# Kernel optimization log

Hardware: AMD Instinct MI355X
Metric: run time of the kernel (lower is better)

## Reference

```python
import jax, jax.numpy as jnp
import numpy as np

N = 50000
H = 300


def l2_normalize(x, eps=1e-12):
    n = jnp.sqrt(jnp.sum(x * x, axis=1, keepdims=True))
    return x / jnp.maximum(n, eps)


def gat_layer(x, ei_j, ei_i, a_i, a_j, n_nodes):
    # per-node scalar scores, gathered per edge
    s_i = x @ a_i  # [N]
    s_j = x @ a_j  # [N]
    e = jax.nn.leaky_relu(s_i[ei_i] + s_j[ei_j], 0.01)  # [E]
    # scatter softmax over incoming edges of node i
    m = jax.ops.segment_max(e, ei_i, num_segments=n_nodes)
    ex = jnp.exp(e - m[ei_i])
    denom = jax.ops.segment_sum(ex, ei_i, num_segments=n_nodes)
    alpha = ex / (denom[ei_i] + 1e-16)
    out = jax.ops.segment_sum(alpha[:, None] * x[ei_j], ei_i, num_segments=n_nodes)
    return jax.nn.relu(out)


def gcn_layer(x, ei_j, ei_i, W, n_nodes):
    deg = jax.ops.segment_sum(jnp.ones_like(ei_i, dtype=x.dtype), ei_i, num_segments=n_nodes)
    dinv = jnp.where(deg > 0, deg ** -0.5, 0.0)
    norm = dinv[ei_j] * dinv[ei_i]  # [E]
    h = x @ W.T
    out = jax.ops.segment_sum(norm[:, None] * h[ei_j], ei_i, num_segments=n_nodes)
    return jax.nn.relu(out)


def highway(x1, x2, W, b):
    gate = jax.nn.sigmoid(x1 @ W.T + b)
    return gate * x2 + (1.0 - gate) * x1


def setup_inputs() -> dict:
    key = jax.random.key(0)
    ks = jax.random.split(key, 16)
    s = 1.0 / np.sqrt(H)
    inp = {
        "x_e": jax.random.normal(ks[0], (N, H), dtype=jnp.float32),
        "edge_index": jax.random.randint(ks[1], (2, 400000), 0, N, dtype=jnp.int32),
        "rel": jax.random.randint(ks[2], (400000,), 0, 1000, dtype=jnp.int32),
        "edge_index_all": jax.random.randint(ks[3], (2, 800000), 0, N, dtype=jnp.int32),
        "rel_all": jax.random.randint(ks[4], (800000,), 0, 1000, dtype=jnp.int32),
        "gcn1_W": jax.random.uniform(ks[5], (H, H), jnp.float32, -s, s),
        "hw1_W": jax.random.uniform(ks[6], (H, H), jnp.float32, -s, s),
        "hw1_b": jax.random.uniform(ks[7], (H,), jnp.float32, -s, s),
        "gat1_ai": jax.random.uniform(ks[8], (H,), jnp.float32, -s, s),
        "gat1_aj": jax.random.uniform(ks[9], (H,), jnp.float32, -s, s),
        "ghw1_W": jax.random.uniform(ks[10], (H, H), jnp.float32, -s, s),
        "ghw1_b": jax.random.uniform(ks[11], (H,), jnp.float32, -s, s),
        "gat2_ai": jax.random.uniform(ks[12], (H,), jnp.float32, -s, s),
        "gat2_aj": jax.random.uniform(ks[13], (H,), jnp.float32, -s, s),
        "ghw2_W": jax.random.uniform(ks[14], (H, H), jnp.float32, -s, s),
        "ghw2_b": jax.random.uniform(ks[15], (H,), jnp.float32, -s, s),
    }
    k2 = jax.random.split(jax.random.key(1), 2)
    inp["gat_ai"] = jax.random.uniform(k2[0], (H,), jnp.float32, -s, s)
    inp["gat_aj"] = jax.random.uniform(k2[1], (H,), jnp.float32, -s, s)
    return inp


def reference(x_e, edge_index, rel, edge_index_all, rel_all,
              gcn1_W, hw1_W, hw1_b, gat1_ai, gat1_aj, ghw1_W, ghw1_b,
              gat2_ai, gat2_aj, ghw2_W, ghw2_b, gat_ai, gat_aj):
    # dropout(p=0.05) treated as identity (eval mode)
    ei_j, ei_i = edge_index_all[0], edge_index_all[1]
    n = x_e.shape[0]

    x0 = l2_normalize(x_e)
    x2 = highway(x0, gcn_layer(x0, ei_j, ei_i, gcn1_W, n), hw1_W, hw1_b)
    x3 = highway(x2, gat_layer(x2, ei_j, ei_i, gat1_ai, gat1_aj, n), ghw1_W, ghw1_b)
    xe = highway(x2, gat_layer(x3, ei_j, ei_i, gat2_ai, gat2_aj, n), ghw2_W, ghw2_b)
    ye = gat_layer(xe, ei_j, ei_i, gat_ai, gat_aj, n)
    return jnp.concatenate([xe, ye], axis=1)
```

## Files before the change

kernel.cpp:

```cpp
#include <hip/hip_runtime.h>
#include <hip/hip_bf16.h>
#include <math.h>

#define H 300
#define WAVE 64
#define STRB 320
#define NCP 20
#define NSS 12
#define ACT 240
#define SCB 1024

typedef short bf16x8 __attribute__((ext_vector_type(8)));
typedef unsigned short u16;
typedef u16 u16x8 __attribute__((ext_vector_type(8)));
typedef u16 u16x4 __attribute__((ext_vector_type(4)));
typedef float f32x4 __attribute__((ext_vector_type(4)));

__device__ inline unsigned short f2b(float f) {
    union { float f; unsigned int u; } x; x.f = f;
    unsigned int r = x.u + 0x7FFF + ((x.u >> 16) & 1);
    return (unsigned short)(r >> 16);
}
__device__ inline float b2f(u16 h) {
    union { float f; unsigned int u; } x; x.u = ((unsigned int)h) << 16;
    return x.f;
}

__global__ void k_l2norm(const float* __restrict__ x, u16* __restrict__ outb, int n) {
    int wave = blockIdx.x * (blockDim.x / WAVE) + (threadIdx.x >> 6);
    int lane = threadIdx.x & 63;
    if (wave >= n) return;
    const float* row = x + (long)wave * H;
    float s = 0.f;
    for (int j = lane; j < H; j += WAVE) { float v = row[j]; s += v * v; }
    for (int o = 32; o > 0; o >>= 1) s += __shfl_xor(s, o);
    float sc = 1.0f / fmaxf(sqrtf(s), 1e-12f);
    u16* brow = outb + (long)wave * STRB;
    for (int j = lane; j < H; j += WAVE) brow[j] = f2b(row[j] * sc);
    for (int j = H + lane; j < STRB; j += WAVE) brow[j] = 0;
}

__global__ void k_zero_int(int* p, int n) {
    int i = blockIdx.x * blockDim.x + threadIdx.x;
    int stride = gridDim.x * blockDim.x;
    for (; i < n; i += stride) p[i] = 0;
}

__global__ void k_count_deg(const int* __restrict__ ei_i, int* __restrict__ deg, int E) {
    int i = blockIdx.x * blockDim.x + threadIdx.x;
    int stride = gridDim.x * blockDim.x;
    for (; i < E; i += stride) atomicAdd(&deg[ei_i[i]], 1);
}

__global__ void k_dinv(const int* __restrict__ deg, float* __restrict__ dinv, int n) {
    int i = blockIdx.x * blockDim.x + threadIdx.x;
    int stride = gridDim.x * blockDim.x;
    for (; i < n; i += stride) {
        int d = deg[i];
        dinv[i] = (d > 0) ? 1.0f / sqrtf((float)d) : 0.0f;
    }
}

__global__ void k_scan_local(const int* __restrict__ deg, int* __restrict__ offs,
                             int* __restrict__ btot, int n) {
    __shared__ int sh[SCB];
    int base = blockIdx.x * SCB;
    int tid = threadIdx.x;
    int v = (base + tid < n) ? deg[base + tid] : 0;
    sh[tid] = v;
    __syncthreads();
    for (int off = 1; off < SCB; off <<= 1) {
        int add = (tid >= off) ? sh[tid - off] : 0;
        __syncthreads();
        sh[tid] += add;
        __syncthreads();
    }
    if (base + tid < n) offs[base + tid] = sh[tid] - v;
    if (tid == SCB - 1) btot[blockIdx.x] = sh[tid];
}

__global__ void k_scan_tots(const int* __restrict__ btot, int* __restrict__ bpre,
                            int nb, int* __restrict__ total_out) {
    int l = threadIdx.x;
    int v = (l < nb) ? btot[l] : 0;
    int own = v;
    for (int o = 1; o < 64; o <<= 1) {
        int u = __shfl_up(v, o);
        if (l >= o) v += u;
    }
    if (l < nb) bpre[l] = v - own;
    if (l == 63) total_out[0] = v;
}

__global__ void k_scan_apply(int* __restrict__ offs, const int* __restrict__ bpre,
                             int* __restrict__ cursor, int n) {
    int i = blockIdx.x * blockDim.x + threadIdx.x;
    int stride = gridDim.x * blockDim.x;
    for (; i < n; i += stride) {
        int o = offs[i] + bpre[i / SCB];
        offs[i] = o;
        cursor[i] = o;
    }
}

__global__ void k_fill_csr(const int* __restrict__ ei_j, const int* __restrict__ ei_i,
                           int* __restrict__ cursor, int* __restrict__ csr_src, int E) {
    int i = blockIdx.x * blockDim.x + threadIdx.x;
    int stride = gridDim.x * blockDim.x;
    for (; i < E; i += stride) {
        int dst = ei_i[i];
        int pos = atomicAdd(&cursor[dst], 1);
        csr_src[pos] = ei_j[i];
    }
}

__global__ void k_conv_w(const float* __restrict__ W, u16* __restrict__ Wb) {
    int idx = blockIdx.x * blockDim.x + threadIdx.x;
    int stride = gridDim.x * blockDim.x;
    for (; idx < STRB * STRB; idx += stride) {
        int r = idx / STRB, c = idx - r * STRB;
        Wb[idx] = (r < H && c < H) ? f2b(W[r * H + c]) : 0;
    }
}

#define BM 128
#define BN 64
#define BK 32
#define LDP 40
#define NXCD 8

__global__ __launch_bounds__(256) void k_gemm_fused(
        const u16* __restrict__ Xb,
        const u16* __restrict__ Wb,
        u16* __restrict__ outb,
        const float* __restrict__ hwbias,
        const u16* __restrict__ xnewb, const float* __restrict__ xnewf,
        const u16* __restrict__ xold,
        float* __restrict__ outf, long ostride,
        u16* __restrict__ mirror,
        int n_rows) {
    __shared__ __align__(16) short As[BM * LDP];
    __shared__ __align__(16) short Bs[BN * LDP];
    const int tid = threadIdx.x;

    const int nwg = gridDim.x;
    const int q = nwg / NXCD, r = nwg % NXCD;
    const int xcd = blockIdx.x % NXCD, idx = blockIdx.x / NXCD;
    const int wgid = (xcd < r ? xcd * (q + 1) : r * (q + 1) + (xcd - r) * q) + idx;
    const int bm = (wgid / 5) * BM;
    const int bn = (wgid % 5) * BN;

    const int lane = tid & 63;
    const int wid = tid >> 6;
    const int wr = wid >> 1;
    const int wc = wid & 1;
    const int lrow = lane & 15;
    const int kgrp = lane >> 4;

    f32x4 acc[4][2];
    #pragma unroll
    for (int m = 0; m < 4; m++)
        #pragma unroll
        for (int n = 0; n < 2; n++) acc[m][n] = (f32x4){0.f, 0.f, 0.f, 0.f};

    for (int k0 = 0; k0 < STRB; k0 += BK) {
        #pragma unroll
        for (int i = 0; i < 2; ++i) {
            int qq = tid + i * 256;
            int rr = qq >> 2, c = (qq & 3) << 3;
            int gr = bm + rr;
            u16x8 v = {0, 0, 0, 0, 0, 0, 0, 0};
            if (gr < n_rows) v = *(const u16x8*)&Xb[(long)gr * STRB + k0 + c];
            *(u16x8*)&As[rr * LDP + c] = v;
        }
        {
            int rr = tid >> 2, c = (tid & 3) << 3;
            u16x8 v = *(const u16x8*)&Wb[(long)(bn + rr) * STRB + k0 + c];
            *(u16x8*)&Bs[rr * LDP + c] = v;
        }
        __syncthreads();

        bf16x8 af[4], bfr[2];
        #pragma unroll
        for (int m = 0; m < 4; m++) {
            int row = wr * 64 + m * 16 + lrow;
            af[m] = *(const bf16x8*)&As[row * LDP + kgrp * 8];
        }
        #pragma unroll
        for (int n = 0; n < 2; n++) {
            int col = wc * 32 + n * 16 + lrow;
            bfr[n] = *(const bf16x8*)&Bs[col * LDP + kgrp * 8];
        }
        #pragma unroll
        for (int m = 0; m < 4; m++)
            #pragma unroll
            for (int n = 0; n < 2; n++)
                acc[m][n] = __builtin_amdgcn_mfma_f32_16x16x32_bf16(af[m], bfr[n], acc[m][n], 0, 0, 0);
        __syncthreads();
    }

    if (outb) {
        #pragma unroll
        for (int m = 0; m < 4; m++)
            #pragma unroll
            for (int n = 0; n < 2; n++) {
                int gc = bn + wc * 32 + n * 16 + lrow;
                if (gc >= STRB) continue;
                #pragma unroll
                for (int rr = 0; rr < 4; rr++) {
                    int gr = bm + wr * 64 + m * 16 + kgrp * 4 + rr;
                    if (gr < n_rows) outb[(long)gr * STRB + gc] = (gc < H) ? f2b(acc[m][n][rr]) : 0;
                }
            }
    } else {
        #pragma unroll
        for (int m = 0; m < 4; m++)
            #pragma unroll
            for (int n = 0; n < 2; n++) {
                int gc = bn + wc * 32 + n * 16 + lrow;
                if (gc >= STRB) continue;
                bool colv = (gc < H);
                float bb = colv ? hwbias[gc] : 0.f;
                #pragma unroll
                for (int rr = 0; rr < 4; rr++) {
                    int gr = bm + wr * 64 + m * 16 + kgrp * 4 + rr;
                    if (gr >= n_rows) continue;
                    if (colv) {
                        float pre = acc[m][n][rr] + bb;
                        float g = 1.0f / (1.0f + __expf(-pre));
                        float xn = xnewb ? b2f(xnewb[(long)gr * STRB + gc])
                                         : xnewf[(long)gr * H + gc];
                        float xo = b2f(xold[(long)gr * STRB + gc]);
                        float val = g * xn + (1.0f - g) * xo;
                        if (outf) outf[(long)gr * ostride + gc] = val;
                        if (mirror) mirror[(long)gr * STRB + gc] = f2b(val);
                    } else if (mirror) {
                        mirror[(long)gr * STRB + gc] = 0;
                    }
                }
            }
    }
}

__global__ __launch_bounds__(256) void k_gcn_gather_b(const u16* __restrict__ xb,
                                                      const float* __restrict__ dinv,
                                                      const int* __restrict__ offs,
                                                      const int* __restrict__ csr,
                                                      u16* __restrict__ outb) {
    int i = blockIdx.x;
    int t = threadIdx.x;
    int esub = t / NCP;
    int cp = t - esub * NCP;
    bool active = (t < ACT);
    int start = offs[i], end = offs[i + 1];
    __shared__ float wsh[256];
    __shared__ int ssh[256];
    __shared__ float redbuf[NSS * STRB];
    float accv[16];
    #pragma unroll
    for (int j = 0; j < 16; j++) accv[j] = 0.f;
    float di = dinv[i];
    for (int cbase = start; cbase < end; cbase += 256) {
        int p = cbase + t;
        if (p < end) {
            int src = csr[p];
            ssh[t] = src;
            wsh[t] = di * dinv[src];
        }
        __syncthreads();
        int cnt = min(256, end - cbase);
        if (active) {
            for (int q = esub; q < cnt; q += NSS) {
                float w = wsh[q];
                const u16* row = xb + (long)ssh[q] * STRB + cp * 16;
                u16x8 v0 = *(const u16x8*)row;
                u16x8 v1 = *(const u16x8*)(row + 8);
                #pragma unroll
                for (int j = 0; j < 8; j++) accv[j] += w * b2f(v0[j]);
                #pragma unroll
                for (int j = 0; j < 8; j++) accv[8 + j] += w * b2f(v1[j]);
            }
        }
        __syncthreads();
    }
    if (active) {
        #pragma unroll
        for (int j = 0; j < 16; j++) redbuf[esub * STRB + cp * 16 + j] = accv[j];
    }
    __syncthreads();
    u16* orow = outb + (long)i * STRB;
    for (int c = t; c < STRB; c += 256) {
        float s = 0.f;
        if (c < H) {
            #pragma unroll
            for (int k = 0; k < NSS; k++) s += redbuf[k * STRB + c];
            s = fmaxf(s, 0.f);
        }
        orow[c] = f2b(s);
    }
}

__global__ void k_dual_dot_b(const u16* __restrict__ xb,
                             const float* __restrict__ ai, const float* __restrict__ aj,
                             float* __restrict__ s_i, float* __restrict__ s_j, int n) {
    int wave = blockIdx.x * (blockDim.x / WAVE) + (threadIdx.x >> 6);
    int lane = threadIdx.x & 63;
    if (wave >= n) return;
    const u16* row = xb + (long)wave * STRB;
    float d0 = 0.f, d1 = 0.f;
    {
        u16x4 v = *(const u16x4*)&row[lane * 4];
        float4 a4 = *(const float4*)&ai[lane * 4];
        float4 j4 = *(const float4*)&aj[lane * 4];
        float x0 = b2f(v[0]), x1 = b2f(v[1]), x2 = b2f(v[2]), x3 = b2f(v[3]);
        d0 = x0 * a4.x + x1 * a4.y + x2 * a4.z + x3 * a4.w;
        d1 = x0 * j4.x + x1 * j4.y + x2 * j4.z + x3 * j4.w;
    }
    if (lane < 11) {
        u16x4 v = *(const u16x4*)&row[256 + lane * 4];
        float4 a4 = *(const float4*)&ai[256 + lane * 4];
        float4 j4 = *(const float4*)&aj[256 + lane * 4];
        float x0 = b2f(v[0]), x1 = b2f(v[1]), x2 = b2f(v[2]), x3 = b2f(v[3]);
        d0 += x0 * a4.x + x1 * a4.y + x2 * a4.z + x3 * a4.w;
        d1 += x0 * j4.x + x1 * j4.y + x2 * j4.z + x3 * j4.w;
    }
    for (int o = 32; o > 0; o >>= 1) { d0 += __shfl_down(d0, o); d1 += __shfl_down(d1, o); }
    if (lane == 0) { s_i[wave] = d0; s_j[wave] = d1; }
}

__global__ __launch_bounds__(256) void k_gat_gather_b(const u16* __restrict__ xb,
                                                      const float* __restrict__ s_i_arr,
                                                      const float* __restrict__ s_j_arr,
                                                      const int* __restrict__ offs,
                                                      const int* __restrict__ csr,
                                                      u16* __restrict__ outb16,
                                                      float* __restrict__ outf, long out_stride,
                                                      int out_off) {
    int i = blockIdx.x;
    int t = threadIdx.x;
    int esub = t / NCP;
    int cp = t - esub * NCP;
    bool active = (t < ACT);
    int start = offs[i], end = offs[i + 1];
    int deg = end - start;
    __shared__ float wsh[256];
    __shared__ int ssh[256];
    __shared__ float redm[256];
    __shared__ float reds[256];
    __shared__ float redbuf[NSS * STRB];
    float accv[16];
    #pragma unroll
    for (int j = 0; j < 16; j++) accv[j] = 0.f;

    if (deg > 0) {
        float si = s_i_arr[i];
        if (deg <= 64) {
            if (t < 64) {
                float sc = 0.f;
                if (t < deg) {
                    int src = csr[start + t];
                    ssh[t] = src;
                    sc = si + s_j_arr[src];
                    sc = (sc >= 0.f) ? sc : 0.01f * sc;
                }
                float mm = (t < deg) ? sc : -1e30f;
                for (int o = 32; o > 0; o >>= 1) mm = fmaxf(mm, __shfl_xor(mm, o));
                float ex = (t < deg) ? __expf(sc - mm) : 0.f;
                float ss = ex;
                for (int o = 32; o > 0; o >>= 1) ss += __shfl_xor(ss, o);
                if (t < deg) wsh[t] = ex / (ss + 1e-16f);
            }
            __syncthreads();
            if (active) {
                for (int q = esub; q < deg; q += NSS) {
                    float w = wsh[q];
                    const u16* row = xb + (long)ssh[q] * STRB + cp * 16;
                    u16x8 v0 = *(const u16x8*)row;
                    u16x8 v1 = *(const u16x8*)(row + 8);
                    #pragma unroll
                    for (int j = 0; j < 8; j++) accv[j] += w * b2f(v0[j]);
                    #pragma unroll
                    for (int j = 0; j < 8; j++) accv[8 + j] += w * b2f(v1[j]);
                }
            }
        } else if (deg <= 256) {
            float sc = 0.f;
            float m_t = -1e30f, s_t = 0.f;
            if (t < deg) {
                int src = csr[start + t];
                sc = si + s_j_arr[src];
                sc = (sc >= 0.f) ? sc : 0.01f * sc;
                m_t = sc; s_t = 1.0f;
                ssh[t] = src;
            }
            redm[t] = m_t; reds[t] = s_t;
            __syncthreads();
            for (int o = 128; o > 0; o >>= 1) {
                if (t < o) {
                    float m1 = redm[t], m2 = redm[t + o];
                    float mm = fmaxf(m1, m2);
                    reds[t] = reds[t] * __expf(m1 - mm) + reds[t + o] * __expf(m2 - mm);
                    redm[t] = mm;
                }
                __syncthreads();
            }
            float m = redm[0];
            float inv = 1.0f / (reds[0] + 1e-16f);
            if (t < deg) wsh[t] = __expf(sc - m) * inv;
            __syncthreads();
            if (active) {
                for (int q = esub; q < deg; q += NSS) {
                    float w = wsh[q];
                    const u16* row = xb + (long)ssh[q] * STRB + cp * 16;
                    u16x8 v0 = *(const u16x8*)row;
                    u16x8 v1 = *(const u16x8*)(row + 8);
                    #pragma unroll
                    for (int j = 0; j < 8; j++) accv[j] += w * b2f(v0[j]);
                    #pragma unroll
                    for (int j = 0; j < 8; j++) accv[8 + j] += w * b2f(v1[j]);
                }
            }
        } else {
            float m_t = -1e30f, s_t = 0.f;
            for (int p = start + t; p < end; p += 256) {
                float sc = si + s_j_arr[csr[p]];
                sc = (sc >= 0.f) ? sc : 0.01f * sc;
                if (sc > m_t) { s_t = s_t * __expf(m_t - sc) + 1.0f; m_t = sc; }
                else s_t += __expf(sc - m_t);
            }
            redm[t] = m_t; reds[t] = s_t;
            __syncthreads();
            for (int o = 128; o > 0; o >>= 1) {
                if (t < o) {
                    float m1 = redm[t], m2 = redm[t + o];
                    float mm = fmaxf(m1, m2);
                    reds[t] = reds[t] * __expf(m1 - mm) + reds[t + o] * __expf(m2 - mm);
                    redm[t] = mm;
                }
                __syncthreads();
            }
            float m = redm[0];
            float inv = 1.0f / (reds[0] + 1e-16f);
            __syncthreads();
            for (int cbase = start; cbase < end; cbase += 256) {
                int p = cbase + t;
                if (p < end) {
                    int src = csr[p];
                    float sc = si + s_j_arr[src];
                    sc = (sc >= 0.f) ? sc : 0.01f * sc;
                    ssh[t] = src;
                    wsh[t] = __expf(sc - m) * inv;
                }
                __syncthreads();
                int cnt = min(256, end - cbase);
                if (active) {
                    for (int q = esub; q < cnt; q += NSS) {
                        float w = wsh[q];
                        const u16* row = xb + (long)ssh[q] * STRB + cp * 16;
                        u16x8 v0 = *(const u16x8*)row;
                        u16x8 v1 = *(const u16x8*)(row + 8);
                        #pragma unroll
                        for (int j = 0; j < 8; j++) accv[j] += w * b2f(v0[j]);
                        #pragma unroll
                        for (int j = 0; j < 8; j++) accv[8 + j] += w * b2f(v1[j]);
                    }
                }
                __syncthreads();
            }
        }
    }
    if (active) {
        #pragma unroll
        for (int j = 0; j < 16; j++) redbuf[esub * STRB + cp * 16 + j] = accv[j];
    }
    __syncthreads();
    if (outb16) {
        u16* orow = outb16 + (long)i * STRB;
        for (int c = t; c < STRB; c += 256) {
            float s = 0.f;
            if (c < H) {
                #pragma unroll
                for (int k = 0; k < NSS; k++) s += redbuf[k * STRB + c];
                s = fmaxf(s, 0.f);
            }
            orow[c] = f2b(s);
        }
    } else {
        for (int c = t; c < H; c += 256) {
            float s = 0.f;
            #pragma unroll
            for (int k = 0; k < NSS; k++) s += redbuf[k * STRB + c];
            outf[(long)i * out_stride + out_off + c] = fmaxf(s, 0.f);
        }
    }
}

extern "C" void kernel_launch(void* const* d_in, const int* in_sizes, int n_in,
                              void* d_out, int out_size, void* d_ws, size_t ws_size,
                              hipStream_t stream) {
    const float* x_e     = (const float*)d_in[0];
    const int*   ei_all  = (const int*)d_in[3];
    const float* gcn1_W  = (const float*)d_in[5];
    const float* hw1_W   = (const float*)d_in[6];
    const float* hw1_b   = (const float*)d_in[7];
    const float* gat1_ai = (const float*)d_in[8];
    const float* gat1_aj = (const float*)d_in[9];
    const float* ghw1_W  = (const float*)d_in[10];
    const float* ghw1_b  = (const float*)d_in[11];
    const float* gat2_ai = (const float*)d_in[12];
    const float* gat2_aj = (const float*)d_in[13];
    const float* ghw2_W  = (const float*)d_in[14];
    const float* ghw2_b  = (const float*)d_in[15];
    const float* gat_ai  = (const float*)d_in[16];
    const float* gat_aj  = (const float*)d_in[17];

    const int N = in_sizes[0] / H;
    const int E = in_sizes[3] / 2;
    const int* ei_j = ei_all;
    const int* ei_i = ei_all + E;

    float* out = (float*)d_out;

    size_t NSB = (size_t)N * STRB;
    u16*   W0   = (u16*)d_ws;
    u16*   W1   = W0 + NSB;
    u16*   W2   = W1 + NSB;
    u16*   W3   = W2 + NSB;
    float* G2F  = (float*)d_ws;
    float* sbi  = (float*)(W3 + NSB);
    float* sbj  = sbi + N;
    float* dinv = sbj + N;
    int*   deg  = (int*)(dinv + N);
    int*   offs = deg + N;
    int*   cursor = offs + (N + 1);
    int*   csr  = cursor + N;
    int*   btot = csr + E;
    int*   bpre = btot + 64;
    u16*   wb0  = (u16*)(bpre + 64);
    u16*   wb1  = wb0 + STRB * STRB;
    u16*   wb2  = wb1 + STRB * STRB;
    u16*   wb3  = wb2 + STRB * STRB;

    dim3 blk256(256);
    int rowsPerBlock = 256 / WAVE;
    dim3 gridRows((N + rowsPerBlock - 1) / rowsPerBlock);
    dim3 gridNode(N);
    dim3 gridE(2048);
    dim3 gridW(100);
    dim3 gridGemm(((N + BM - 1) / BM) * 5);
    int nScanB = (N + SCB - 1) / SCB;

    hipLaunchKernelGGL(k_l2norm, gridRows, blk256, 0, stream, x_e, W0, N);

    hipLaunchKernelGGL(k_zero_int, dim3(256), blk256, 0, stream, deg, N);
    hipLaunchKernelGGL(k_count_deg, gridE, blk256, 0, stream, ei_i, deg, E);
    hipLaunchKernelGGL(k_dinv, dim3(256), blk256, 0, stream, deg, dinv, N);
    hipLaunchKernelGGL(k_scan_local, dim3(nScanB), dim3(SCB), 0, stream, deg, offs, btot, N);
    hipLaunchKernelGGL(k_scan_tots, dim3(1), dim3(64), 0, stream, btot, bpre, nScanB, offs + N);
    hipLaunchKernelGGL(k_scan_apply, dim3(256), blk256, 0, stream, offs, bpre, cursor, N);
    hipLaunchKernelGGL(k_fill_csr, gridE, blk256, 0, stream, ei_j, ei_i, cursor, csr, E);
    hipLaunchKernelGGL(k_conv_w, gridW, blk256, 0, stream, gcn1_W, wb0);
    hipLaunchKernelGGL(k_conv_w, gridW, blk256, 0, stream, hw1_W, wb1);
    hipLaunchKernelGGL(k_conv_w, gridW, blk256, 0, stream, ghw1_W, wb2);
    hipLaunchKernelGGL(k_conv_w, gridW, blk256, 0, stream, ghw2_W, wb3);

    hipLaunchKernelGGL(k_gemm_fused, gridGemm, blk256, 0, stream,
                       W0, wb0, W1,
                       (const float*)nullptr, (const u16*)nullptr, (const float*)nullptr,
                       (const u16*)nullptr, (float*)nullptr, (long)0, (u16*)nullptr, N);

    hipLaunchKernelGGL(k_gcn_gather_b, gridNode, blk256, 0, stream, W1, dinv, offs, csr, W2);

    hipLaunchKernelGGL(k_gemm_fused, gridGemm, blk256, 0, stream,
                       W0, wb1, (u16*)nullptr,
                       hw1_b, W2, (const float*)nullptr, W0,
                       (float*)nullptr, (long)0, W3, N);

    hipLaunchKernelGGL(k_dual_dot_b, gridRows, blk256, 0, stream, W3, gat1_ai, gat1_aj, sbi, sbj, N);

    hipLaunchKernelGGL(k_gat_gather_b, gridNode, blk256, 0, stream, W3, sbi, sbj, offs, csr,
                       W1, (float*)nullptr, (long)0, 0);

    hipLaunchKernelGGL(k_gemm_fused, gridGemm, blk256, 0, stream,
                       W3, wb2, (u16*)nullptr,
                       ghw1_b, W1, (const float*)nullptr, W3,
                       (float*)nullptr, (long)0, W2, N);

    hipLaunchKernelGGL(k_dual_dot_b, gridRows, blk256, 0, stream, W2, gat2_ai, gat2_aj, sbi, sbj, N);

    hipLaunchKernelGGL(k_gat_gather_b, gridNode, blk256, 0, stream, W2, sbi, sbj, offs, csr,
                       (u16*)nullptr, G2F, (long)H, 0);

    hipLaunchKernelGGL(k_gemm_fused, gridGemm, blk256, 0, stream,
                       W3, wb3, (u16*)nullptr,
                       ghw2_b, (const u16*)nullptr, G2F, W3,
                       out, (long)(2 * H), W2, N);

    hipLaunchKernelGGL(k_dual_dot_b, gridRows, blk256, 0, stream, W2, gat_ai, gat_aj, sbi, sbj, N);

    hipLaunchKernelGGL(k_gat_gather_b, gridNode, blk256, 0, stream, W2, sbi, sbj, offs, csr,
                       (u16*)nullptr, out, (long)(2 * H), H);
}
```

Measured before the change: 809.8 us.

## Switch node gathers to one wavefront per node; merge weight conversions

Replaces the block-per-node GCN and GAT gather kernels, which used shared memory, block barriers and a cross-subgroup reduction, with a wave-per-node design. Four nodes share each 256-thread block, edge indices and weights are broadcast with shuffles, and each of 40 lanes accumulates 8 columns in registers. The GAT softmax now uses a single-wave online max/sum reduction in place of the degree-dependent block paths. The four weight-conversion launches are merged into one kernel. With an average degree near 16, this removes the barrier overhead and idle threads, but each edge row is now fetched one at a time per wave, which limits memory-level parallelism.

```diff
diff --git a/kernel.cpp b/kernel.cpp
--- a/kernel.cpp
+++ b/kernel.cpp
@@ -5,9 +5,6 @@
 #define H 300
 #define WAVE 64
 #define STRB 320
-#define NCP 20
-#define NSS 12
-#define ACT 240
 #define SCB 1024
 
 typedef short bf16x8 __attribute__((ext_vector_type(8)));
@@ -114,9 +111,15 @@
     }
 }
 
-__global__ void k_conv_w(const float* __restrict__ W, u16* __restrict__ Wb) {
-    int idx = blockIdx.x * blockDim.x + threadIdx.x;
-    int stride = gridDim.x * blockDim.x;
+__global__ void k_conv_w4(const float* __restrict__ W0f, const float* __restrict__ W1f,
+                          const float* __restrict__ W2f, const float* __restrict__ W3f,
+                          u16* __restrict__ Wb0, u16* __restrict__ Wb1,
+                          u16* __restrict__ Wb2, u16* __restrict__ Wb3) {
+    int which = blockIdx.x & 3;
+    const float* W = (which == 0) ? W0f : (which == 1) ? W1f : (which == 2) ? W2f : W3f;
+    u16* Wb = (which == 0) ? Wb0 : (which == 1) ? Wb1 : (which == 2) ? Wb2 : Wb3;
+    int idx = (blockIdx.x >> 2) * blockDim.x + threadIdx.x;
+    int stride = (gridDim.x >> 2) * blockDim.x;
     for (; idx < STRB * STRB; idx += stride) {
         int r = idx / STRB, c = idx - r * STRB;
         Wb[idx] = (r < H && c < H) ? f2b(W[r * H + c]) : 0;
@@ -242,61 +245,42 @@
     }
 }
 
-__global__ __launch_bounds__(256) void k_gcn_gather_b(const u16* __restrict__ xb,
+__global__ __launch_bounds__(256) void k_gcn_gather_w(const u16* __restrict__ xb,
                                                       const float* __restrict__ dinv,
                                                       const int* __restrict__ offs,
                                                       const int* __restrict__ csr,
-                                                      u16* __restrict__ outb) {
-    int i = blockIdx.x;
-    int t = threadIdx.x;
-    int esub = t / NCP;
-    int cp = t - esub * NCP;
-    bool active = (t < ACT);
-    int start = offs[i], end = offs[i + 1];
-    __shared__ float wsh[256];
-    __shared__ int ssh[256];
-    __shared__ float redbuf[NSS * STRB];
-    float accv[16];
+                                                      u16* __restrict__ outb, int n) {
+    int node = blockIdx.x * 4 + (threadIdx.x >> 6);
+    int lane = threadIdx.x & 63;
+    if (node >= n) return;
+    int start = offs[node], end = offs[node + 1];
+    float acc[8];
     #pragma unroll
-    for (int j = 0; j < 16; j++) accv[j] = 0.f;
-    float di = dinv[i];
-    for (int cbase = start; cbase < end; cbase += 256) {
-        int p = cbase + t;
+    for (int j = 0; j < 8; j++) acc[j] = 0.f;
+    float di = dinv[node];
+    for (int tb = start; tb < end; tb += 64) {
+        int p = tb + lane;
+        int src = 0; float w = 0.f;
         if (p < end) {
-            int src = csr[p];
-            ssh[t] = src;
-            wsh[t] = di * dinv[src];
-        }
-        __syncthreads();
-        int cnt = min(256, end - cbase);
-        if (active) {
-            for (int q = esub; q < cnt; q += NSS) {
-                float w = wsh[q];
-                const u16* row = xb + (long)ssh[q] * STRB + cp * 16;
-                u16x8 v0 = *(const u16x8*)row;
-                u16x8 v1 = *(const u16x8*)(row + 8);
+            src = csr[p];
+            w = di * dinv[src];
+        }
+        int cnt = min(64, end - tb);
+        for (int qq = 0; qq < cnt; qq++) {
+            float wq = __shfl(w, qq);
+            int sq = __shfl(src, qq);
+            if (lane < 40) {
+                u16x8 v = *(const u16x8*)&xb[(long)sq * STRB + lane * 8];
                 #pragma unroll
-                for (int j = 0; j < 8; j++) accv[j] += w * b2f(v0[j]);
-                #pragma unroll
-                for (int j = 0; j < 8; j++) accv[8 + j] += w * b2f(v1[j]);
-            }
-        }
-        __syncthreads();
-    }
-    if (active) {
-        #pragma unroll
-        for (int j = 0; j < 16; j++) redbuf[esub * STRB + cp * 16 + j] = accv[j];
-    }
-    __syncthreads();
-    u16* orow = outb + (long)i * STRB;
-    for (int c = t; c < STRB; c += 256) {
-        float s = 0.f;
-        if (c < H) {
-            #pragma unroll
-            for (int k = 0; k < NSS; k++) s += redbuf[k * STRB + c];
-            s = fmaxf(s, 0.f);
-        }
-        orow[c] = f2b(s);
+                for (int j = 0; j < 8; j++) acc[j] += wq * b2f(v[j]);
+            }
+        }
+    }
+    if (lane < 40) {
+        u16x8 o;
+        #pragma unroll
+        for (int j = 0; j < 8; j++) o[j] = f2b(fmaxf(acc[j], 0.f));
+        *(u16x8*)&outb[(long)node * STRB + lane * 8] = o;
     }
 }
 
@@ -328,169 +312,75 @@
     if (lane == 0) { s_i[wave] = d0; s_j[wave] = d1; }
 }
 
-__global__ __launch_bounds__(256) void k_gat_gather_b(const u16* __restrict__ xb,
+__global__ __launch_bounds__(256) void k_gat_gather_w(const u16* __restrict__ xb,
                                                       const float* __restrict__ s_i_arr,
                                                       const float* __restrict__ s_j_arr,
                                                       const int* __restrict__ offs,
                                                       const int* __restrict__ csr,
                                                       u16* __restrict__ outb16,
                                                       float* __restrict__ outf, long out_stride,
-                                                      int out_off) {
-    int i = blockIdx.x;
-    int t = threadIdx.x;
-    int esub = t / NCP;
-    int cp = t - esub * NCP;
-    bool active = (t < ACT);
-    int start = offs[i], end = offs[i + 1];
+                                                      int out_off, int n) {
+    int node = blockIdx.x * 4 + (threadIdx.x >> 6);
+    int lane = threadIdx.x & 63;
+    if (node >= n) return;
+    int start = offs[node], end = offs[node + 1];
     int deg = end - start;
-    __shared__ float wsh[256];
-    __shared__ int ssh[256];
-    __shared__ float redm[256];
-    __shared__ float reds[256];
-    __shared__ float redbuf[NSS * STRB];
-    float accv[16];
+    float acc[8];
     #pragma unroll
-    for (int j = 0; j < 16; j++) accv[j] = 0.f;
+    for (int j = 0; j < 8; j++) acc[j] = 0.f;
 
     if (deg > 0) {
-        float si = s_i_arr[i];
-        if (deg <= 64) {
-            if (t < 64) {
-                float sc = 0.f;
-                if (t < deg) {
-                    int src = csr[start + t];
-                    ssh[t] = src;
-                    sc = si + s_j_arr[src];
-                    sc = (sc >= 0.f) ? sc : 0.01f * sc;
+        float si = s_i_arr[node];
+        float m_t = -1e30f, s_t = 0.f;
+        for (int p = start + lane; p < end; p += 64) {
+            float sc = si + s_j_arr[csr[p]];
+            sc = (sc >= 0.f) ? sc : 0.01f * sc;
+            if (sc > m_t) { s_t = s_t * __expf(m_t - sc) + 1.0f; m_t = sc; }
+            else s_t += __expf(sc - m_t);
+        }
+        for (int o = 32; o > 0; o >>= 1) {
+            float m2 = __shfl_xor(m_t, o), s2 = __shfl_xor(s_t, o);
+            float mm = fmaxf(m_t, m2);
+            s_t = s_t * __expf(m_t - mm) + s2 * __expf(m2 - mm);
+            m_t = mm;
+        }
+        float m = m_t;
+        float inv = 1.0f / (s_t + 1e-16f);
+        for (int tb = start; tb < end; tb += 64) {
+            int p = tb + lane;
+            int src = 0; float w = 0.f;
+            if (p < end) {
+                src = csr[p];
+                float sc = si + s_j_arr[src];
+                sc = (sc >= 0.f) ? sc : 0.01f * sc;
+                w = __expf(sc - m) * inv;
+            }
+            int cnt = min(64, end - tb);
+            for (int qq = 0; qq < cnt; qq++) {
+                float wq = __shfl(w, qq);
+                int sq = __shfl(src, qq);
+                if (lane < 40) {
+                    u16x8 v = *(const u16x8*)&xb[(long)sq * STRB + lane * 8];
+                    #pragma unroll
+                    for (int j = 0; j < 8; j++) acc[j] += wq * b2f(v[j]);
                 }
-                float mm = (t < deg) ? sc : -1e30f;
-                for (int o = 32; o > 0; o >>= 1) mm = fmaxf(mm, __shfl_xor(mm, o));
-                float ex = (t < deg) ? __expf(sc - mm) : 0.f;
-                float ss = ex;
-                for (int o = 32; o > 0; o >>= 1) ss += __shfl_xor(ss, o);
-                if (t < deg) wsh[t] = ex / (ss + 1e-16f);
-            }
-            __syncthreads();
-            if (active) {
-                for (int q = esub; q < deg; q += NSS) {
-                    float w = wsh[q];
-                    const u16* row = xb + (long)ssh[q] * STRB + cp * 16;
-                    u16x8 v0 = *(const u16x8*)row;
-                    u16x8 v1 = *(const u16x8*)(row + 8);
-                    #pragma unroll
-                    for (int j = 0; j < 8; j++) accv[j] += w * b2f(v0[j]);
-                    #pragma unroll
-                    for (int j = 0; j < 8; j++) accv[8 + j] += w * b2f(v1[j]);
-                }
-            }
-        } else if (deg <= 256) {
-            float sc = 0.f;
-            float m_t = -1e30f, s_t = 0.f;
-            if (t < deg) {
-                int src = csr[start + t];
-                sc = si + s_j_arr[src];
-                sc = (sc >= 0.f) ? sc : 0.01f * sc;
-                m_t = sc; s_t = 1.0f;
-                ssh[t] = src;
-            }
-            redm[t] = m_t; reds[t] = s_t;
-            __syncthreads();
-            for (int o = 128; o > 0; o >>= 1) {
-                if (t < o) {
-                    float m1 = redm[t], m2 = redm[t + o];
-                    float mm = fmaxf(m1, m2);
-                    reds[t] = reds[t] * __expf(m1 - mm) + reds[t + o] * __expf(m2 - mm);
-                    redm[t] = mm;
-                }
-                __syncthreads();
-            }
-            float m = redm[0];
-            float inv = 1.0f / (reds[0] + 1e-16f);
-            if (t < deg) wsh[t] = __expf(sc - m) * inv;
-            __syncthreads();
-            if (active) {
-                for (int q = esub; q < deg; q += NSS) {
-                    float w = wsh[q];
-                    const u16* row = xb + (long)ssh[q] * STRB + cp * 16;
-                    u16x8 v0 = *(const u16x8*)row;
-                    u16x8 v1 = *(const u16x8*)(row + 8);
-                    #pragma unroll
-                    for (int j = 0; j < 8; j++) accv[j] += w * b2f(v0[j]);
-                    #pragma unroll
-                    for (int j = 0; j < 8; j++) accv[8 + j] += w * b2f(v1[j]);
-                }
-            }
-        } else {
-            float m_t = -1e30f, s_t = 0.f;
-            for (int p = start + t; p < end; p += 256) {
-                float sc = si + s_j_arr[csr[p]];
-                sc = (sc >= 0.f) ? sc : 0.01f * sc;
-                if (sc > m_t) { s_t = s_t * __expf(m_t - sc) + 1.0f; m_t = sc; }
-                else s_t += __expf(sc - m_t);
-            }
-            redm[t] = m_t; reds[t] = s_t;
-            __syncthreads();
-            for (int o = 128; o > 0; o >>= 1) {
-                if (t < o) {
-                    float m1 = redm[t], m2 = redm[t + o];
-                    float mm = fmaxf(m1, m2);
-                    reds[t] = reds[t] * __expf(m1 - mm) + reds[t + o] * __expf(m2 - mm);
-                    redm[t] = mm;
-                }
-                __syncthreads();
-            }
-            float m = redm[0];
-            float inv = 1.0f / (reds[0] + 1e-16f);
-            __syncthreads();
-            for (int cbase = start; cbase < end; cbase += 256) {
-                int p = cbase + t;
-                if (p < end) {
-                    int src = csr[p];
-                    float sc = si + s_j_arr[src];
-                    sc = (sc >= 0.f) ? sc : 0.01f * sc;
-                    ssh[t] = src;
-                    wsh[t] = __expf(sc - m) * inv;
-                }
-                __syncthreads();
-                int cnt = min(256, end - cbase);
-                if (active) {
-                    for (int q = esub; q < cnt; q += NSS) {
-                        float w = wsh[q];
-                        const u16* row = xb + (long)ssh[q] * STRB + cp * 16;
-                        u16x8 v0 = *(const u16x8*)row;
-                        u16x8 v1 = *(const u16x8*)(row + 8);
-                        #pragma unroll
-                        for (int j = 0; j < 8; j++) accv[j] += w * b2f(v0[j]);
-                        #pragma unroll
-                        for (int j = 0; j < 8; j++) accv[8 + j] += w * b2f(v1[j]);
-                    }
-                }
-                __syncthreads();
-            }
-        }
-    }
-    if (active) {
-        #pragma unroll
-        for (int j = 0; j < 16; j++) redbuf[esub * STRB + cp * 16 + j] = accv[j];
-    }
-    __syncthreads();
+            }
+        }
+    }
     if (outb16) {
-        u16* orow = outb16 + (long)i * STRB;
-        for (int c = t; c < STRB; c += 256) {
-            float s = 0.f;
-            if (c < H) {
-                #pragma unroll
-                for (int k = 0; k < NSS; k++) s += redbuf[k * STRB + c];
-                s = fmaxf(s, 0.f);
-            }
-            orow[c] = f2b(s);
+        if (lane < 40) {
+            u16x8 o;
+            #pragma unroll
+            for (int j = 0; j < 8; j++) o[j] = f2b(fmaxf(acc[j], 0.f));
+            *(u16x8*)&outb16[(long)node * STRB + lane * 8] = o;
         }
     } else {
-        for (int c = t; c < H; c += 256) {
-            float s = 0.f;
+        if (lane < 38) {
             #pragma unroll
-            for (int k = 0; k < NSS; k++) s += redbuf[k * STRB + c];
-            outf[(long)i * out_stride + out_off + c] = fmaxf(s, 0.f);
+            for (int j = 0; j < 8; j++) {
+                int c = lane * 8 + j;
+                if (c < H) outf[(long)node * out_stride + out_off + c] = fmaxf(acc[j], 0.f);
+            }
         }
     }
 }
@@ -544,9 +434,9 @@
     dim3 blk256(256);
     int rowsPerBlock = 256 / WAVE;
     dim3 gridRows((N + rowsPerBlock - 1) / rowsPerBlock);
-    dim3 gridNode(N);
+    dim3 gridNodeW((N + 3) / 4);
     dim3 gridE(2048);
-    dim3 gridW(100);
+    dim3 gridW(400);
     dim3 gridGemm(((N + BM - 1) / BM) * 5);
     int nScanB = (N + SCB - 1) / SCB;
 
@@ -559,17 +449,15 @@
     hipLaunchKernelGGL(k_scan_tots, dim3(1), dim3(64), 0, stream, btot, bpre, nScanB, offs + N);
     hipLaunchKernelGGL(k_scan_apply, dim3(256), blk256, 0, stream, offs, bpre, cursor, N);
     hipLaunchKernelGGL(k_fill_csr, gridE, blk256, 0, stream, ei_j, ei_i, cursor, csr, E);
-    hipLaunchKernelGGL(k_conv_w, gridW, blk256, 0, stream, gcn1_W, wb0);
-    hipLaunchKernelGGL(k_conv_w, gridW, blk256, 0, stream, hw1_W, wb1);
-    hipLaunchKernelGGL(k_conv_w, gridW, blk256, 0, stream, ghw1_W, wb2);
-    hipLaunchKernelGGL(k_conv_w, gridW, blk256, 0, stream, ghw2_W, wb3);
+    hipLaunchKernelGGL(k_conv_w4, gridW, blk256, 0, stream,
+                       gcn1_W, hw1_W, ghw1_W, ghw2_W, wb0, wb1, wb2, wb3);
 
     hipLaunchKernelGGL(k_gemm_fused, gridGemm, blk256, 0, stream,
                        W0, wb0, W1,
                        (const float*)nullptr, (const u16*)nullptr, (const float*)nullptr,
                        (const u16*)nullptr, (float*)nullptr, (long)0, (u16*)nullptr, N);
 
-    hipLaunchKernelGGL(k_gcn_gather_b, gridNode, blk256, 0, stream, W1, dinv, offs, csr, W2);
+    hipLaunchKernelGGL(k_gcn_gather_w, gridNodeW, blk256, 0, stream, W1, dinv, offs, csr, W2, N);
 
     hipLaunchKernelGGL(k_gemm_fused, gridGemm, blk256, 0, stream,
                        W0, wb1, (u16*)nullptr,
@@ -578,8 +466,8 @@
 
     hipLaunchKernelGGL(k_dual_dot_b, gridRows, blk256, 0, stream, W3, gat1_ai, gat1_aj, sbi, sbj, N);
 
-    hipLaunchKernelGGL(k_gat_gather_b, gridNode, blk256, 0, stream, W3, sbi, sbj, offs, csr,
-                       W1, (float*)nullptr, (long)0, 0);
+    hipLaunchKernelGGL(k_gat_gather_w, gridNodeW, blk256, 0, stream, W3, sbi, sbj, offs, csr,
+                       W1, (float*)nullptr, (long)0, 0, N);
 
     hipLaunchKernelGGL(k_gemm_fused, gridGemm, blk256, 0, stream,
                        W3, wb2, (u16*)nullptr,
@@ -588,8 +476,8 @@
 
     hipLaunchKernelGGL(k_dual_dot_b, gridRows, blk256, 0, stream, W2, gat2_ai, gat2_aj, sbi, sbj, N);
 
-    hipLaunchKernelGGL(k_gat_gather_b, gridNode, blk256, 0, stream, W2, sbi, sbj, offs, csr,
-                       (u16*)nullptr, G2F, (long)H, 0);
+    hipLaunchKernelGGL(k_gat_gather_w, gridNodeW, blk256, 0, stream, W2, sbi, sbj, offs, csr,
+                       (u16*)nullptr, G2F, (long)H, 0, N);
 
     hipLaunchKernelGGL(k_gemm_fused, gridGemm, blk256, 0, stream,
                        W3, wb3, (u16*)nullptr,
@@ -598,6 +486,6 @@
 
     hipLaunchKernelGGL(k_dual_dot_b, gridRows, blk256, 0, stream, W2, gat_ai, gat_aj, sbi, sbj, N);
 
-    hipLaunchKernelGGL(k_gat_gather_b, gridNode, blk256, 0, stream, W2, sbi, sbj, offs, csr,
-                       (u16*)nullptr, out, (long)(2 * H), H);
-}
+    hipLaunchKernelGGL(k_gat_gather_w, gridNodeW, blk256, 0, stream, W2, sbi, sbj, offs, csr,
+                       (u16*)nullptr, out, (long)(2 * H), H, N);
+}
```

Result: faster. 743.6 us (-8.2%).
